# Performance work log

Hardware: AMD Instinct MI355X
Metric: run time of the kernel (lower is better)

The kernel has to match this reference:

```python
import jax, jax.numpy as jnp
import numpy as np

NUM_TOKENS = 16384
DIM = 4096
N_EXPERTS = 256
ROUTE_SCALE = 1.0


def setup_inputs() -> dict:
    key = jax.random.key(0)
    k_x, k_w = jax.random.split(key)
    x = jax.random.normal(k_x, (NUM_TOKENS, DIM), dtype=jnp.float32)
    # nn.init.normal_(weight, std=0.02)
    weight = 0.02 * jax.random.normal(k_w, (N_EXPERTS, DIM), dtype=jnp.float32)
    return {"x": x, "weight": weight}


def reference(x, weight):
    # Router GEMM: [T, D] @ [D, E] -> [T, E]
    scores = jnp.einsum("td,ed->te", x, weight)
    # Eval-mode token_choice path: softmax in fp32
    probs = jax.nn.softmax(scores.astype(jnp.float32), axis=-1)  # [T, E]
    indices = jnp.argmax(probs, axis=-1, keepdims=True)  # [T, 1] int
    # Hard one-hot scatter of argmax
    y_hard = jax.nn.one_hot(indices[:, 0], N_EXPERTS, dtype=probs.dtype)  # [T, E]
    # Straight-through estimator mix
    ste = jax.lax.stop_gradient(y_hard - probs) + probs
    # Gather routing weight at the selected expert
    weights = jnp.take_along_axis(ste, indices, axis=-1)  # [T, 1]
    weights = (weights * ROUTE_SCALE).astype(x.dtype)
    return weights, indices
```

## Files before the change

kernel.cpp:

```cpp
#include <hip/hip_runtime.h>
#include <stdint.h>

#define NUM_TOKENS 16384
#define DIM        4096
#define NEXP       256
#define MB         32
#define BK         64
#define NITER      (DIM / BK)
#define APAD       72
#define NWAVES     4
#define MARGIN     0.025f
#define CAP        16384

typedef __attribute__((ext_vector_type(4))) float   f32x4;
typedef __attribute__((ext_vector_type(8))) __bf16  bf16x8;
typedef __attribute__((ext_vector_type(8))) unsigned short u16x8;

static __device__ __forceinline__ unsigned short f32_to_bf16(float f) {
    unsigned int u = __float_as_uint(f);
    u += 0x7fffu + ((u >> 16) & 1u);
    return (unsigned short)(u >> 16);
}

__global__ void cvt_weights(const float* __restrict__ w,
                            unsigned short* __restrict__ wh,
                            int* __restrict__ counter) {
    if (blockIdx.x == 0 && threadIdx.x == 0) *counter = 0;
    const int n4 = NEXP * DIM / 4;
    const int stride = gridDim.x * blockDim.x;
    for (int i = blockIdx.x * blockDim.x + threadIdx.x; i < n4; i += stride) {
        float4 v = ((const float4*)w)[i];
        ushort4 h;
        h.x = f32_to_bf16(v.x); h.y = f32_to_bf16(v.y);
        h.z = f32_to_bf16(v.z); h.w = f32_to_bf16(v.w);
        ((ushort4*)wh)[i] = h;
    }
}

__global__ __launch_bounds__(256, 4) void gate_main(
    const float* __restrict__ x,
    const unsigned short* __restrict__ wh,
    float* __restrict__ out,
    int* __restrict__ counter,
    int4* __restrict__ entries)
{
    __shared__ unsigned short lAh[MB][APAD];
    __shared__ unsigned short lBh[NEXP * BK];
    __shared__ float4 cand[NWAVES][MB];

    const int tid  = threadIdx.x;
    const int wv   = tid >> 6;
    const int lane = tid & 63;
    const int tok0 = blockIdx.x * MB;

    const int ta   = tid >> 3;
    const int kseg = (tid & 7) * 8;
    const float* xrow = x + (size_t)(tok0 + ta) * DIM + kseg;

    const int esub   = lane >> 3;
    const int bk_off = ((lane & 7) ^ esub) * 8;

    const int quad = lane >> 4;
    const int col  = lane & 15;

    f32x4 acc[2][4];
    #pragma unroll
    for (int mt = 0; mt < 2; ++mt)
        #pragma unroll
        for (int nt = 0; nt < 4; ++nt)
            acc[mt][nt] = f32x4{0.f, 0.f, 0.f, 0.f};

    float4 xv0 = *(const float4*)(xrow);
    float4 xv1 = *(const float4*)(xrow + 4);

    for (int it = 0; it < NITER; ++it) {
        const int k0 = it * BK;

        #pragma unroll
        for (int jj = 0; jj < 8; ++jj) {
            const int e = wv * 64 + jj * 8 + esub;
            const unsigned short* gh = wh + (size_t)e * DIM + k0 + bk_off;
            unsigned short* dh = &lBh[(wv * 64 + jj * 8) * BK];
            __builtin_amdgcn_global_load_lds(
                (const __attribute__((address_space(1))) unsigned int*)gh,
                (__attribute__((address_space(3))) unsigned int*)dh, 16, 0, 0);
        }

        {
            u16x8 h0;
            h0[0] = f32_to_bf16(xv0.x); h0[1] = f32_to_bf16(xv0.y);
            h0[2] = f32_to_bf16(xv0.z); h0[3] = f32_to_bf16(xv0.w);
            h0[4] = f32_to_bf16(xv1.x); h0[5] = f32_to_bf16(xv1.y);
            h0[6] = f32_to_bf16(xv1.z); h0[7] = f32_to_bf16(xv1.w);
            *(u16x8*)&lAh[ta][kseg] = h0;
        }
        __syncthreads();

        if (it + 1 < NITER) {
            xv0 = *(const float4*)(xrow + (it + 1) * BK);
            xv1 = *(const float4*)(xrow + (it + 1) * BK + 4);
        }

        #pragma unroll
        for (int kk = 0; kk < BK; kk += 32) {
            const int kc = kk >> 3;
            bf16x8 ah[2], bh[4];
            #pragma unroll
            for (int mt = 0; mt < 2; ++mt)
                ah[mt] = *(const bf16x8*)&lAh[mt * 16 + col][kk + quad * 8];
            #pragma unroll
            for (int nt = 0; nt < 4; ++nt) {
                const int e = wv * 64 + nt * 16 + col;
                const int cpos = (((kc + quad) ^ (col & 7)) * 8);
                bh[nt] = *(const bf16x8*)&lBh[e * BK + cpos];
            }
            #pragma unroll
            for (int mt = 0; mt < 2; ++mt)
                #pragma unroll
                for (int nt = 0; nt < 4; ++nt)
                    acc[mt][nt] = __builtin_amdgcn_mfma_f32_16x16x32_bf16(
                        ah[mt], bh[nt], acc[mt][nt], 0, 0, 0);
        }
        __syncthreads();
    }

    #pragma unroll
    for (int mt = 0; mt < 2; ++mt) {
        #pragma unroll
        for (int r = 0; r < 4; ++r) {
            float t1s = acc[mt][0][r]; int t1e = wv * 64 + col;
            float t2s = acc[mt][1][r]; int t2e = t1e + 16;
            if (t2s > t1s) { float ts = t1s; int te = t1e; t1s = t2s; t1e = t2e; t2s = ts; t2e = te; }
            #pragma unroll
            for (int nt = 2; nt < 4; ++nt) {
                float s = acc[mt][nt][r]; int e = wv * 64 + nt * 16 + col;
                if (s > t1s)      { t2s = t1s; t2e = t1e; t1s = s; t1e = e; }
                else if (s > t2s) { t2s = s; t2e = e; }
            }
            #pragma unroll
            for (int m = 1; m <= 8; m <<= 1) {
                float o1s = __shfl_xor(t1s, m); int o1e = __shfl_xor(t1e, m);
                float o2s = __shfl_xor(t2s, m); int o2e = __shfl_xor(t2e, m);
                bool o1_top = (o1s > t1s) || (o1s == t1s && o1e < t1e);
                if (o1_top) {
                    bool keep_t1 = (t1s > o2s) || (t1s == o2s && t1e < o2e);
                    t2s = keep_t1 ? t1s : o2s; t2e = keep_t1 ? t1e : o2e;
                    t1s = o1s; t1e = o1e;
                } else {
                    bool o1_2nd = (o1s > t2s) || (o1s == t2s && o1e < t2e);
                    if (o1_2nd) { t2s = o1s; t2e = o1e; }
                }
            }
            if (col == 0) {
                int tok = mt * 16 + quad * 4 + r;
                cand[wv][tok] = make_float4(t1s, __int_as_float(t1e), t2s, __int_as_float(t2e));
            }
        }
    }
    __syncthreads();

    if (tid < MB) {
        float4 c0 = cand[0][tid];
        float t1s = c0.x; int t1e = __float_as_int(c0.y);
        float t2s = c0.z; int t2e = __float_as_int(c0.w);
        #pragma unroll
        for (int wvi = 1; wvi < NWAVES; ++wvi) {
            float4 c = cand[wvi][tid];
            float o1s = c.x; int o1e = __float_as_int(c.y);
            float o2s = c.z; int o2e = __float_as_int(c.w);
            bool o1_top = (o1s > t1s) || (o1s == t1s && o1e < t1e);
            if (o1_top) {
                bool keep_t1 = (t1s > o2s) || (t1s == o2s && t1e < o2e);
                t2s = keep_t1 ? t1s : o2s; t2e = keep_t1 ? t1e : o2e;
                t1s = o1s; t1e = o1e;
            } else {
                bool o1_2nd = (o1s > t2s) || (o1s == t2s && o1e < t2e);
                if (o1_2nd) { t2s = o1s; t2e = o1e; }
            }
        }
        const int gtok = tok0 + tid;
        out[gtok] = 1.0f;
        out[NUM_TOKENS + gtok] = (float)t1e;
        if (t1s - t2s < MARGIN) {
            int slot = atomicAdd(counter, 1);
            if (slot < CAP) entries[slot] = make_int4(gtok, t1e, t2e, 0);
        }
    }
}

__global__ void refine(const float* __restrict__ x,
                       const float* __restrict__ w,
                       const int* __restrict__ counter,
                       const int4* __restrict__ entries,
                       float* __restrict__ out) {
    const int gwave  = (blockIdx.x * blockDim.x + threadIdx.x) >> 6;
    const int lane   = threadIdx.x & 63;
    const int nwaves = (gridDim.x * blockDim.x) >> 6;
    int n = *counter; if (n > CAP) n = CAP;
    for (int i = gwave; i < n; i += nwaves) {
        int4 e = entries[i];
        const float* xr = x + (size_t)e.x * DIM;
        const float* w1 = w + (size_t)e.y * DIM;
        const float* w2 = w + (size_t)e.z * DIM;
        double d1 = 0.0, d2 = 0.0;
        for (int k = lane; k < DIM; k += 64) {
            double xv = (double)xr[k];
            d1 += xv * (double)w1[k];
            d2 += xv * (double)w2[k];
        }
        #pragma unroll
        for (int m = 32; m > 0; m >>= 1) {
            d1 += __shfl_xor(d1, m);
            d2 += __shfl_xor(d2, m);
        }
        if (lane == 0) {
            int best = (d1 > d2) ? e.y : ((d2 > d1) ? e.z : (e.y < e.z ? e.y : e.z));
            out[NUM_TOKENS + e.x] = (float)best;
        }
    }
}

extern "C" void kernel_launch(void* const* d_in, const int* in_sizes, int n_in,
                              void* d_out, int out_size, void* d_ws, size_t ws_size,
                              hipStream_t stream) {
    const float* x = (const float*)d_in[0];
    const float* w = (const float*)d_in[1];
    float* out = (float*)d_out;

    char* ws = (char*)d_ws;
    unsigned short* wh = (unsigned short*)ws;
    int*  counter = (int*)(ws + (2u << 20));
    int4* entries = (int4*)(ws + (2u << 20) + 16);

    cvt_weights<<<256, 256, 0, stream>>>(w, wh, counter);
    gate_main<<<NUM_TOKENS / MB, 256, 0, stream>>>(x, wh, out, counter, entries);
    refine<<<256, 256, 0, stream>>>(x, w, counter, entries, out);
}
```

Measured before the change: 437.4 us.

## Prepack weights into MFMA fragment layout and drop LDS staging

Weights are converted to bf16 in a layout matching MFMA B fragments, so each wave loads them straight from global memory. The A tile is read directly from x per lane instead of being staged through LDS. This removes all shared-memory staging and the per-iteration barriers. The trade-off is heavier L2 traffic for the weights and no explicit software prefetch of x.

```diff
diff --git a/kernel.cpp b/kernel.cpp
--- a/kernel.cpp
+++ b/kernel.cpp
@@ -1,67 +1,63 @@
 #include <hip/hip_runtime.h>
+#include <hip/hip_bf16.h>
 #include <stdint.h>
 
 #define NUM_TOKENS 16384
 #define DIM        4096
 #define NEXP       256
 #define MB         32
-#define BK         64
-#define NITER      (DIM / BK)
-#define APAD       72
+#define NKB        (DIM / 32)
 #define NWAVES     4
 #define MARGIN     0.025f
 #define CAP        16384
 
 typedef __attribute__((ext_vector_type(4))) float   f32x4;
 typedef __attribute__((ext_vector_type(8))) __bf16  bf16x8;
-typedef __attribute__((ext_vector_type(8))) unsigned short u16x8;
 
-static __device__ __forceinline__ unsigned short f32_to_bf16(float f) {
-    unsigned int u = __float_as_uint(f);
-    u += 0x7fffu + ((u >> 16) & 1u);
-    return (unsigned short)(u >> 16);
+static __device__ __forceinline__ bf16x8 pack8(float4 u, float4 v) {
+    union { bf16x8 v8; __hip_bfloat162 h[4]; } r;
+    r.h[0] = __float22bfloat162_rn(float2{u.x, u.y});
+    r.h[1] = __float22bfloat162_rn(float2{u.z, u.w});
+    r.h[2] = __float22bfloat162_rn(float2{v.x, v.y});
+    r.h[3] = __float22bfloat162_rn(float2{v.z, v.w});
+    return r.v8;
 }
 
-__global__ void cvt_weights(const float* __restrict__ w,
-                            unsigned short* __restrict__ wh,
-                            int* __restrict__ counter) {
+__global__ void pack_weights(const float* __restrict__ w,
+                             __hip_bfloat16* __restrict__ P,
+                             int* __restrict__ counter) {
     if (blockIdx.x == 0 && threadIdx.x == 0) *counter = 0;
-    const int n4 = NEXP * DIM / 4;
-    const int stride = gridDim.x * blockDim.x;
-    for (int i = blockIdx.x * blockDim.x + threadIdx.x; i < n4; i += stride) {
-        float4 v = ((const float4*)w)[i];
-        ushort4 h;
-        h.x = f32_to_bf16(v.x); h.y = f32_to_bf16(v.y);
-        h.z = f32_to_bf16(v.z); h.w = f32_to_bf16(v.w);
-        ((ushort4*)wh)[i] = h;
-    }
+    const int gid  = blockIdx.x * blockDim.x + threadIdx.x;
+    const int kb   = gid >> 10;
+    const int rem  = gid & 1023;
+    const int g    = rem >> 6;
+    const int lane = rem & 63;
+    const int e    = g * 16 + (lane & 15);
+    const int k    = kb * 32 + (lane >> 4) * 8;
+    const float4 u = *(const float4*)(w + (size_t)e * DIM + k);
+    const float4 v = *(const float4*)(w + (size_t)e * DIM + k + 4);
+    *(bf16x8*)(P + (size_t)gid * 8) = pack8(u, v);
 }
 
 __global__ __launch_bounds__(256, 4) void gate_main(
     const float* __restrict__ x,
-    const unsigned short* __restrict__ wh,
+    const __hip_bfloat16* __restrict__ P,
     float* __restrict__ out,
     int* __restrict__ counter,
     int4* __restrict__ entries)
 {
-    __shared__ unsigned short lAh[MB][APAD];
-    __shared__ unsigned short lBh[NEXP * BK];
     __shared__ float4 cand[NWAVES][MB];
 
     const int tid  = threadIdx.x;
     const int wv   = tid >> 6;
     const int lane = tid & 63;
+    const int quad = lane >> 4;
+    const int col  = lane & 15;
     const int tok0 = blockIdx.x * MB;
 
-    const int ta   = tid >> 3;
-    const int kseg = (tid & 7) * 8;
-    const float* xrow = x + (size_t)(tok0 + ta) * DIM + kseg;
-
-    const int esub   = lane >> 3;
-    const int bk_off = ((lane & 7) ^ esub) * 8;
-
-    const int quad = lane >> 4;
-    const int col  = lane & 15;
+    const float* xr0 = x + (size_t)(tok0 + col) * DIM + quad * 8;
+    const float* xr1 = x + (size_t)(tok0 + 16 + col) * DIM + quad * 8;
+    const __hip_bfloat16* Pw = P + (size_t)(wv * 4) * 512 + (size_t)lane * 8;
 
     f32x4 acc[2][4];
     #pragma unroll
@@ -70,58 +66,23 @@
         for (int nt = 0; nt < 4; ++nt)
             acc[mt][nt] = f32x4{0.f, 0.f, 0.f, 0.f};
 
-    float4 xv0 = *(const float4*)(xrow);
-    float4 xv1 = *(const float4*)(xrow + 4);
-
-    for (int it = 0; it < NITER; ++it) {
-        const int k0 = it * BK;
-
+    for (int kb = 0; kb < NKB; ++kb) {
+        const int koff = kb * 32;
+        float4 a00 = *(const float4*)(xr0 + koff);
+        float4 a01 = *(const float4*)(xr0 + koff + 4);
+        float4 a10 = *(const float4*)(xr1 + koff);
+        float4 a11 = *(const float4*)(xr1 + koff + 4);
+        bf16x8 bh[4];
         #pragma unroll
-        for (int jj = 0; jj < 8; ++jj) {
-            const int e = wv * 64 + jj * 8 + esub;
-            const unsigned short* gh = wh + (size_t)e * DIM + k0 + bk_off;
-            unsigned short* dh = &lBh[(wv * 64 + jj * 8) * BK];
-            __builtin_amdgcn_global_load_lds(
-                (const __attribute__((address_space(1))) unsigned int*)gh,
-                (__attribute__((address_space(3))) unsigned int*)dh, 16, 0, 0);
+        for (int nt = 0; nt < 4; ++nt)
+            bh[nt] = *(const bf16x8*)(Pw + (size_t)kb * 8192 + nt * 512);
+        bf16x8 ah0 = pack8(a00, a01);
+        bf16x8 ah1 = pack8(a10, a11);
+        #pragma unroll
+        for (int nt = 0; nt < 4; ++nt) {
+            acc[0][nt] = __builtin_amdgcn_mfma_f32_16x16x32_bf16(ah0, bh[nt], acc[0][nt], 0, 0, 0);
+            acc[1][nt] = __builtin_amdgcn_mfma_f32_16x16x32_bf16(ah1, bh[nt], acc[1][nt], 0, 0, 0);
         }
-
-        {
-            u16x8 h0;
-            h0[0] = f32_to_bf16(xv0.x); h0[1] = f32_to_bf16(xv0.y);
-            h0[2] = f32_to_bf16(xv0.z); h0[3] = f32_to_bf16(xv0.w);
-            h0[4] = f32_to_bf16(xv1.x); h0[5] = f32_to_bf16(xv1.y);
-            h0[6] = f32_to_bf16(xv1.z); h0[7] = f32_to_bf16(xv1.w);
-            *(u16x8*)&lAh[ta][kseg] = h0;
-        }
-        __syncthreads();
-
-        if (it + 1 < NITER) {
-            xv0 = *(const float4*)(xrow + (it + 1) * BK);
-            xv1 = *(const float4*)(xrow + (it + 1) * BK + 4);
-        }
-
-        #pragma unroll
-        for (int kk = 0; kk < BK; kk += 32) {
-            const int kc = kk >> 3;
-            bf16x8 ah[2], bh[4];
-            #pragma unroll
-            for (int mt = 0; mt < 2; ++mt)
-                ah[mt] = *(const bf16x8*)&lAh[mt * 16 + col][kk + quad * 8];
-            #pragma unroll
-            for (int nt = 0; nt < 4; ++nt) {
-                const int e = wv * 64 + nt * 16 + col;
-                const int cpos = (((kc + quad) ^ (col & 7)) * 8);
-                bh[nt] = *(const bf16x8*)&lBh[e * BK + cpos];
-            }
-            #pragma unroll
-            for (int mt = 0; mt < 2; ++mt)
-                #pragma unroll
-                for (int nt = 0; nt < 4; ++nt)
-                    acc[mt][nt] = __builtin_amdgcn_mfma_f32_16x16x32_bf16(
-                        ah[mt], bh[nt], acc[mt][nt], 0, 0, 0);
-        }
-        __syncthreads();
     }
 
     #pragma unroll
@@ -228,11 +189,11 @@
     float* out = (float*)d_out;
 
     char* ws = (char*)d_ws;
-    unsigned short* wh = (unsigned short*)ws;
+    __hip_bfloat16* P = (__hip_bfloat16*)ws;
     int*  counter = (int*)(ws + (2u << 20));
     int4* entries = (int4*)(ws + (2u << 20) + 16);
 
-    cvt_weights<<<256, 256, 0, stream>>>(w, wh, counter);
-    gate_main<<<NUM_TOKENS / MB, 256, 0, stream>>>(x, wh, out, counter, entries);
+    pack_weights<<<NKB * 16 * 64 / 256, 256, 0, stream>>>(w, P, counter);
+    gate_main<<<NUM_TOKENS / MB, 256, 0, stream>>>(x, P, out, counter, entries);
     refine<<<256, 256, 0, stream>>>(x, w, counter, entries, out);
 }
```

Measured after the change: 536.6 us. 1.23x slower.
